# Optimization experiments

Measured on AMD Instinct MI355X. Metric: run time of the kernel, lower is better.

The kernel has to match this reference:

```python
import jax, jax.numpy as jnp
import numpy as np

IN1, IN2, OUT = 256, 64, 64

def setup_inputs() -> dict:
    key = jax.random.key(0)
    k1, k2, k3, k4 = jax.random.split(key, 4)
    x1 = jax.random.normal(k1, (4, 4096, IN1), dtype=jnp.float32)
    x2 = jax.random.normal(k2, (4, 4096, IN2), dtype=jnp.float32)
    # nn.Linear(in_1, in_2*out): weight (in_2*out, in_1), bias (in_2*out,)
    W = jax.random.normal(k3, (IN2 * OUT, IN1), dtype=jnp.float32) / np.sqrt(IN1)
    bvec = jax.random.normal(k4, (IN2 * OUT,), dtype=jnp.float32) * 0.01
    return {"x1": x1, "x2": x2, "W": W, "bvec": bvec}

def reference(x1, x2, W, bvec):
    b, n, _ = x1.shape
    # per-token generated weight: (b, n, in_2, out)
    w = (jnp.einsum('bni,oi->bno', x1, W) + bvec).reshape(b, n, IN2, OUT)
    # batched vector-matrix product per token
    y = jnp.einsum('bnj,bnjo->bno', x2, w)
    return y
```

## Files before the change

kernel.cpp:

```cpp
#include <hip/hip_runtime.h>


#define FRAGS 16
#define FRAG_SHORTS 512
#define JF_SHORTS (FRAGS * FRAG_SHORTS)
#define BIAS_OFF ((size_t)(64 * 2 * FRAGS) * FRAG_SHORTS)

typedef __bf16 bf16x8 __attribute__((ext_vector_type(8)));
typedef float  f32x16 __attribute__((ext_vector_type(16)));

static __device__ __forceinline__ unsigned short f2bf(float f) {
  union { float f; unsigned u; } v; v.f = f;
  unsigned r = v.u + 0x7FFFu + ((v.u >> 16) & 1u);
  return (unsigned short)(r >> 16);
}

static __device__ __forceinline__ void gload_lds16(const unsigned short* g,
                                                   unsigned short* l) {
  __builtin_amdgcn_global_load_lds(
      (const __attribute__((address_space(1))) void*)g,
      (__attribute__((address_space(3))) void*)l, 16, 0, 0);
}

__global__ void prep_w(const float* __restrict__ W, const float* __restrict__ bv,
                       unsigned short* __restrict__ Wf) {
  int idx = blockIdx.x * 256 + threadIdx.x;
  int r  = idx >> 4;
  int ks = idx & 15;
  int j   = r >> 6;
  int o   = r & 63;
  int oh  = o >> 5;
  int l31 = o & 31;
  size_t fb = ((size_t)(j * 2 + oh) * FRAGS + ks) * FRAG_SHORTS;

  const float4* row = (const float4*)(W + (size_t)r * 256 + ks * 16);
  float4 v0 = row[0], v1 = row[1], v2 = row[2], v3 = row[3];
  ushort4 lo0, lo1, hi0, hi1;
  lo0.x = f2bf(v0.x); lo0.y = f2bf(v0.y); lo0.z = f2bf(v0.z); lo0.w = f2bf(v0.w);
  lo1.x = f2bf(v1.x); lo1.y = f2bf(v1.y); lo1.z = f2bf(v1.z); lo1.w = f2bf(v1.w);
  hi0.x = f2bf(v2.x); hi0.y = f2bf(v2.y); hi0.z = f2bf(v2.z); hi0.w = f2bf(v2.w);
  hi1.x = f2bf(v3.x); hi1.y = f2bf(v3.y); hi1.z = f2bf(v3.z); hi1.w = f2bf(v3.w);
  *(ushort4*)&Wf[fb + l31 * 8 + 0] = lo0;
  *(ushort4*)&Wf[fb + l31 * 8 + 4] = lo1;
  *(ushort4*)&Wf[fb + 256 + l31 * 8 + 0] = hi0;
  *(ushort4*)&Wf[fb + 256 + l31 * 8 + 4] = hi1;

  if (idx < 512) {
    int f   = idx >> 6;
    int ln  = idx & 63;
    int ohb = f >> 2, jhb = f & 3;
    int lb  = ln & 31, lgb = ln >> 5;
    #pragma unroll
    for (int e = 0; e < 8; ++e)
      Wf[BIAS_OFF + (size_t)f * FRAG_SHORTS + ln * 8 + e] =
          f2bf(bv[(jhb * 16 + 8 * lgb + e) * 64 + 32 * ohb + lb]);
  }
}

__global__ __launch_bounds__(512, 2)
void meta_main(const float* __restrict__ x1, const float* __restrict__ x2,
               const unsigned short* __restrict__ Wf, float* __restrict__ out) {
  __shared__ __align__(16) unsigned char smem[163840];
  unsigned short* sWf = (unsigned short*)smem;
  float* sX2 = (float*)(smem + 131072);

  const int tid  = threadIdx.x;
  const int lane = tid & 63;
  const int wv   = tid >> 6;
  const int th   = wv & 1;
  const int jh   = wv >> 1;
  const int l31  = lane & 31;
  const int lg   = lane >> 5;

  const int bid  = blockIdx.x;
  const int xcd  = bid & 7;
  const int kk   = bid >> 3;
  const int tile = xcd * 16 + (kk >> 1);
  const int oh   = kk & 1;
  const long tile0 = (long)tile * 128;

  {
    const float4* src = (const float4*)(x1 + tile0 * 256);
    #pragma unroll
    for (int it = 0; it < 16; ++it) {
      int fi4 = it * 512 + tid;
      float4 v = src[fi4];
      int token = fi4 >> 6;
      int col   = (fi4 & 63) * 4;
      ushort4 b;
      b.x = f2bf(v.x); b.y = f2bf(v.y); b.z = f2bf(v.z); b.w = f2bf(v.w);
      *(ushort4*)&sWf[token * 264 + col] = b;
    }
    const float4* s2 = (const float4*)(x2 + tile0 * 64);
    #pragma unroll
    for (int it = 0; it < 4; ++it) {
      int fi4 = it * 512 + tid;
      float4 v = s2[fi4];
      int token = fi4 >> 4;
      int j0    = (fi4 & 15) * 4;
      sX2[(j0 + 0) * 128 + token] = v.x;
      sX2[(j0 + 1) * 128 + token] = v.y;
      sX2[(j0 + 2) * 128 + token] = v.z;
      sX2[(j0 + 3) * 128 + token] = v.w;
    }
  }
  __syncthreads();

  const int tA = th * 64 + l31;
  const int tB = tA + 32;

  bf16x8 bfA[16], bfB[16];
  #pragma unroll
  for (int ks = 0; ks < 16; ++ks) {
    bfA[ks] = *(const bf16x8*)&sWf[tA * 264 + ks * 16 + lg * 8];
    bfB[ks] = *(const bf16x8*)&sWf[tB * 264 + ks * 16 + lg * 8];
  }

  f32x16 yA, yB;
  {
    union { bf16x8 v; unsigned short u[8]; } xfA, xfB;
    #pragma unroll
    for (int e = 0; e < 8; ++e) {
      int jrow = jh * 16 + 8 * lg + e;
      xfA.u[e] = f2bf(sX2[jrow * 128 + tA]);
      xfB.u[e] = f2bf(sX2[jrow * 128 + tB]);
    }
    bf16x8 biasA = *(const bf16x8*)(Wf + BIAS_OFF +
                                    (size_t)(oh * 4 + jh) * FRAG_SHORTS + lane * 8);
    f32x16 z;
    #pragma unroll
    for (int r2 = 0; r2 < 16; ++r2) z[r2] = 0.0f;
    yA = __builtin_amdgcn_mfma_f32_32x32x16_bf16(biasA, xfA.v, z, 0, 0, 0);
    yB = __builtin_amdgcn_mfma_f32_32x32x16_bf16(biasA, xfB.v, z, 0, 0, 0);
  }
  __syncthreads();

  unsigned short* ring = sWf + jh * (2 * JF_SHORTS);
  const int ks0 = th * 8;

  {
    const unsigned short* src =
        Wf + ((size_t)((jh * 16) * 2 + oh) * FRAGS + ks0) * FRAG_SHORTS + lane * 8;
    unsigned short* dst = ring + ks0 * FRAG_SHORTS;
    #pragma unroll
    for (int q = 0; q < 8; ++q)
      gload_lds16(src + q * FRAG_SHORTS, dst + q * FRAG_SHORTS);
  }
  __syncthreads();

  #pragma unroll 2
  for (int i = 0; i < 16; ++i) {
    const int buf = i & 1;
    if (i + 1 < 16) {
      const int jn = jh * 16 + i + 1;
      const unsigned short* src =
          Wf + ((size_t)(jn * 2 + oh) * FRAGS + ks0) * FRAG_SHORTS + lane * 8;
      unsigned short* dst = ring + (buf ^ 1) * JF_SHORTS + ks0 * FRAG_SHORTS;
      #pragma unroll
      for (int q = 0; q < 8; ++q)
        gload_lds16(src + q * FRAG_SHORTS, dst + q * FRAG_SHORTS);
    }
    const unsigned short* rb = ring + buf * JF_SHORTS + lane * 8;
    f32x16 aA, aB;
    #pragma unroll
    for (int r2 = 0; r2 < 16; ++r2) { aA[r2] = 0.0f; aB[r2] = 0.0f; }
    #pragma unroll
    for (int ks = 0; ks < 16; ++ks) {
      bf16x8 wk = *(const bf16x8*)(rb + ks * FRAG_SHORTS);
      aA = __builtin_amdgcn_mfma_f32_32x32x16_bf16(wk, bfA[ks], aA, 0, 0, 0);
      aB = __builtin_amdgcn_mfma_f32_32x32x16_bf16(wk, bfB[ks], aB, 0, 0, 0);
    }
    const int j = jh * 16 + i;
    const float xA = sX2[j * 128 + tA];
    const float xB = sX2[j * 128 + tB];
    #pragma unroll
    for (int r2 = 0; r2 < 16; ++r2) {
      yA[r2] += xA * aA[r2];
      yB[r2] += xB * aB[r2];
    }
    __syncthreads();
  }

  float* red = (float*)sWf;
  const int sA = ((th * 2 + 0) * 64 + lane) * 4 + jh;
  const int sB = ((th * 2 + 1) * 64 + lane) * 4 + jh;
  if (jh != 0) {
    #pragma unroll
    for (int r2 = 0; r2 < 16; ++r2) {
      red[sA * 17 + r2] = yA[r2];
      red[sB * 17 + r2] = yB[r2];
    }
  }
  __syncthreads();
  if (jh == 0) {
    #pragma unroll
    for (int r2 = 0; r2 < 16; ++r2) {
      yA[r2] += red[(sA + 1) * 17 + r2] + red[(sA + 2) * 17 + r2] + red[(sA + 3) * 17 + r2];
      yB[r2] += red[(sB + 1) * 17 + r2] + red[(sB + 2) * 17 + r2] + red[(sB + 3) * 17 + r2];
    }
    float* yoA = out + (tile0 + tA) * 64 + oh * 32;
    float* yoB = out + (tile0 + tB) * 64 + oh * 32;
    #pragma unroll
    for (int rq = 0; rq < 4; ++rq) {
      float4 vA = make_float4(yA[4 * rq + 0], yA[4 * rq + 1], yA[4 * rq + 2], yA[4 * rq + 3]);
      float4 vB = make_float4(yB[4 * rq + 0], yB[4 * rq + 1], yB[4 * rq + 2], yB[4 * rq + 3]);
      *(float4*)(yoA + 8 * rq + 4 * lg) = vA;
      *(float4*)(yoB + 8 * rq + 4 * lg) = vB;
    }
  }
}

extern "C" void kernel_launch(void* const* d_in, const int* in_sizes, int n_in,
                              void* d_out, int out_size, void* d_ws, size_t ws_size,
                              hipStream_t stream) {
  const float* x1 = (const float*)d_in[0];
  const float* x2 = (const float*)d_in[1];
  const float* W  = (const float*)d_in[2];
  const float* bv = (const float*)d_in[3];
  float* y = (float*)d_out;
  unsigned short* Wf = (unsigned short*)d_ws;

  prep_w<<<256, 256, 0, stream>>>(W, bv, Wf);
  meta_main<<<256, 512, 0, stream>>>(x1, x2, Wf, y);
}
```

Baseline: 105.6 us.

## Split K across waves with register-streamed W fragments and tree reduction

Rewrites the main kernel's work split: each wave now owns a quarter of the K dimension and half of the j range, covering all 128 tokens. It loads x1 fragments straight from global into registers and streams the bf16 W fragments from global with register double-buffering, replacing the LDS ring fed by global_load_lds and its per-iteration barriers. Partial sums are combined through a multi-step LDS tree reduction. The aim is to cut barrier and LDS traffic and reuse each W fragment across more tokens, at the cost of more reduction work, higher register pressure, and dropping the XCD-aware tile mapping.

```diff
diff --git a/kernel.cpp b/kernel.cpp
--- a/kernel.cpp
+++ b/kernel.cpp
@@ -1,10 +1,9 @@
 #include <hip/hip_runtime.h>
 
 
-#define FRAGS 16
 #define FRAG_SHORTS 512
-#define JF_SHORTS (FRAGS * FRAG_SHORTS)
-#define BIAS_OFF ((size_t)(64 * 2 * FRAGS) * FRAG_SHORTS)
+#define JSTEP (2 * 16 * FRAG_SHORTS)
+#define BIAS_OFF ((size_t)(64 * 2 * 16) * FRAG_SHORTS)
 
 typedef __bf16 bf16x8 __attribute__((ext_vector_type(8)));
 typedef float  f32x16 __attribute__((ext_vector_type(16)));
@@ -15,11 +14,11 @@
   return (unsigned short)(r >> 16);
 }
 
-static __device__ __forceinline__ void gload_lds16(const unsigned short* g,
-                                                   unsigned short* l) {
-  __builtin_amdgcn_global_load_lds(
-      (const __attribute__((address_space(1))) void*)g,
-      (__attribute__((address_space(3))) void*)l, 16, 0, 0);
+static __device__ __forceinline__ bf16x8 pack8(float4 a, float4 b) {
+  union { bf16x8 v; unsigned short u[8]; } r;
+  r.u[0] = f2bf(a.x); r.u[1] = f2bf(a.y); r.u[2] = f2bf(a.z); r.u[3] = f2bf(a.w);
+  r.u[4] = f2bf(b.x); r.u[5] = f2bf(b.y); r.u[6] = f2bf(b.z); r.u[7] = f2bf(b.w);
+  return r.v;
 }
 
 __global__ void prep_w(const float* __restrict__ W, const float* __restrict__ bv,
@@ -31,7 +30,7 @@
   int o   = r & 63;
   int oh  = o >> 5;
   int l31 = o & 31;
-  size_t fb = ((size_t)(j * 2 + oh) * FRAGS + ks) * FRAG_SHORTS;
+  size_t fb = ((size_t)(j * 2 + oh) * 16 + ks) * FRAG_SHORTS;
 
   const float4* row = (const float4*)(W + (size_t)r * 256 + ks * 16);
   float4 v0 = row[0], v1 = row[1], v2 = row[2], v3 = row[3];
@@ -48,49 +47,35 @@
   if (idx < 512) {
     int f   = idx >> 6;
     int ln  = idx & 63;
-    int ohb = f >> 2, jhb = f & 3;
+    int ohb = f >> 2, jq = f & 3;
     int lb  = ln & 31, lgb = ln >> 5;
     #pragma unroll
     for (int e = 0; e < 8; ++e)
       Wf[BIAS_OFF + (size_t)f * FRAG_SHORTS + ln * 8 + e] =
-          f2bf(bv[(jhb * 16 + 8 * lgb + e) * 64 + 32 * ohb + lb]);
+          f2bf(bv[(jq * 16 + 8 * lgb + e) * 64 + 32 * ohb + lb]);
   }
 }
 
 __global__ __launch_bounds__(512, 2)
 void meta_main(const float* __restrict__ x1, const float* __restrict__ x2,
                const unsigned short* __restrict__ Wf, float* __restrict__ out) {
-  __shared__ __align__(16) unsigned char smem[163840];
-  unsigned short* sWf = (unsigned short*)smem;
-  float* sX2 = (float*)(smem + 131072);
+  __shared__ __align__(16) unsigned char smem[102400];
+  float* sX2 = (float*)smem;
+  float* red = (float*)(smem + 32768);
 
   const int tid  = threadIdx.x;
   const int lane = tid & 63;
   const int wv   = tid >> 6;
-  const int th   = wv & 1;
-  const int jh   = wv >> 1;
+  const int kh   = wv & 3;
+  const int jh   = wv >> 2;
   const int l31  = lane & 31;
   const int lg   = lane >> 5;
 
   const int bid  = blockIdx.x;
-  const int xcd  = bid & 7;
-  const int kk   = bid >> 3;
-  const int tile = xcd * 16 + (kk >> 1);
-  const int oh   = kk & 1;
-  const long tile0 = (long)tile * 128;
+  const int oh   = bid & 1;
+  const long tile0 = (long)(bid >> 1) * 128;
 
   {
-    const float4* src = (const float4*)(x1 + tile0 * 256);
-    #pragma unroll
-    for (int it = 0; it < 16; ++it) {
-      int fi4 = it * 512 + tid;
-      float4 v = src[fi4];
-      int token = fi4 >> 6;
-      int col   = (fi4 & 63) * 4;
-      ushort4 b;
-      b.x = f2bf(v.x); b.y = f2bf(v.y); b.z = f2bf(v.z); b.w = f2bf(v.w);
-      *(ushort4*)&sWf[token * 264 + col] = b;
-    }
     const float4* s2 = (const float4*)(x2 + tile0 * 64);
     #pragma unroll
     for (int it = 0; it < 4; ++it) {
@@ -104,110 +89,137 @@
       sX2[(j0 + 3) * 128 + token] = v.w;
     }
   }
-  __syncthreads();
-
-  const int tA = th * 64 + l31;
-  const int tB = tA + 32;
-
-  bf16x8 bfA[16], bfB[16];
-  #pragma unroll
-  for (int ks = 0; ks < 16; ++ks) {
-    bfA[ks] = *(const bf16x8*)&sWf[tA * 264 + ks * 16 + lg * 8];
-    bfB[ks] = *(const bf16x8*)&sWf[tB * 264 + ks * 16 + lg * 8];
-  }
-
-  f32x16 yA, yB;
-  {
-    union { bf16x8 v; unsigned short u[8]; } xfA, xfB;
-    #pragma unroll
-    for (int e = 0; e < 8; ++e) {
-      int jrow = jh * 16 + 8 * lg + e;
-      xfA.u[e] = f2bf(sX2[jrow * 128 + tA]);
-      xfB.u[e] = f2bf(sX2[jrow * 128 + tB]);
-    }
-    bf16x8 biasA = *(const bf16x8*)(Wf + BIAS_OFF +
-                                    (size_t)(oh * 4 + jh) * FRAG_SHORTS + lane * 8);
-    f32x16 z;
-    #pragma unroll
-    for (int r2 = 0; r2 < 16; ++r2) z[r2] = 0.0f;
-    yA = __builtin_amdgcn_mfma_f32_32x32x16_bf16(biasA, xfA.v, z, 0, 0, 0);
-    yB = __builtin_amdgcn_mfma_f32_32x32x16_bf16(biasA, xfB.v, z, 0, 0, 0);
-  }
-  __syncthreads();
-
-  unsigned short* ring = sWf + jh * (2 * JF_SHORTS);
-  const int ks0 = th * 8;
-
-  {
-    const unsigned short* src =
-        Wf + ((size_t)((jh * 16) * 2 + oh) * FRAGS + ks0) * FRAG_SHORTS + lane * 8;
-    unsigned short* dst = ring + ks0 * FRAG_SHORTS;
-    #pragma unroll
-    for (int q = 0; q < 8; ++q)
-      gload_lds16(src + q * FRAG_SHORTS, dst + q * FRAG_SHORTS);
-  }
-  __syncthreads();
-
-  #pragma unroll 2
-  for (int i = 0; i < 16; ++i) {
-    const int buf = i & 1;
-    if (i + 1 < 16) {
-      const int jn = jh * 16 + i + 1;
-      const unsigned short* src =
-          Wf + ((size_t)(jn * 2 + oh) * FRAGS + ks0) * FRAG_SHORTS + lane * 8;
-      unsigned short* dst = ring + (buf ^ 1) * JF_SHORTS + ks0 * FRAG_SHORTS;
+
+  bf16x8 bf[4][4];
+  #pragma unroll
+  for (int m = 0; m < 4; ++m) {
+    #pragma unroll
+    for (int q = 0; q < 4; ++q) {
+      const float* p = x1 + (size_t)(tile0 + m * 32 + l31) * 256 +
+                       (kh * 4 + q) * 16 + lg * 8;
+      bf[m][q] = pack8(*(const float4*)p, *(const float4*)(p + 4));
+    }
+  }
+  __syncthreads();
+
+  f32x16 z;
+  #pragma unroll
+  for (int r = 0; r < 16; ++r) z[r] = 0.0f;
+
+  f32x16 y[4];
+  #pragma unroll
+  for (int m = 0; m < 4; ++m) y[m] = z;
+  if (kh == 0) {
+    #pragma unroll
+    for (int qq = 0; qq < 2; ++qq) {
+      int jq = jh * 2 + qq;
+      bf16x8 bias = *(const bf16x8*)(Wf + BIAS_OFF +
+                                     (size_t)(oh * 4 + jq) * FRAG_SHORTS + lane * 8);
       #pragma unroll
-      for (int q = 0; q < 8; ++q)
-        gload_lds16(src + q * FRAG_SHORTS, dst + q * FRAG_SHORTS);
-    }
-    const unsigned short* rb = ring + buf * JF_SHORTS + lane * 8;
-    f32x16 aA, aB;
-    #pragma unroll
-    for (int r2 = 0; r2 < 16; ++r2) { aA[r2] = 0.0f; aB[r2] = 0.0f; }
-    #pragma unroll
-    for (int ks = 0; ks < 16; ++ks) {
-      bf16x8 wk = *(const bf16x8*)(rb + ks * FRAG_SHORTS);
-      aA = __builtin_amdgcn_mfma_f32_32x32x16_bf16(wk, bfA[ks], aA, 0, 0, 0);
-      aB = __builtin_amdgcn_mfma_f32_32x32x16_bf16(wk, bfB[ks], aB, 0, 0, 0);
-    }
-    const int j = jh * 16 + i;
-    const float xA = sX2[j * 128 + tA];
-    const float xB = sX2[j * 128 + tB];
-    #pragma unroll
-    for (int r2 = 0; r2 < 16; ++r2) {
-      yA[r2] += xA * aA[r2];
-      yB[r2] += xB * aB[r2];
-    }
-    __syncthreads();
-  }
-
-  float* red = (float*)sWf;
-  const int sA = ((th * 2 + 0) * 64 + lane) * 4 + jh;
-  const int sB = ((th * 2 + 1) * 64 + lane) * 4 + jh;
-  if (jh != 0) {
-    #pragma unroll
-    for (int r2 = 0; r2 < 16; ++r2) {
-      red[sA * 17 + r2] = yA[r2];
-      red[sB * 17 + r2] = yB[r2];
-    }
-  }
-  __syncthreads();
-  if (jh == 0) {
-    #pragma unroll
-    for (int r2 = 0; r2 < 16; ++r2) {
-      yA[r2] += red[(sA + 1) * 17 + r2] + red[(sA + 2) * 17 + r2] + red[(sA + 3) * 17 + r2];
-      yB[r2] += red[(sB + 1) * 17 + r2] + red[(sB + 2) * 17 + r2] + red[(sB + 3) * 17 + r2];
-    }
-    float* yoA = out + (tile0 + tA) * 64 + oh * 32;
-    float* yoB = out + (tile0 + tB) * 64 + oh * 32;
-    #pragma unroll
-    for (int rq = 0; rq < 4; ++rq) {
-      float4 vA = make_float4(yA[4 * rq + 0], yA[4 * rq + 1], yA[4 * rq + 2], yA[4 * rq + 3]);
-      float4 vB = make_float4(yB[4 * rq + 0], yB[4 * rq + 1], yB[4 * rq + 2], yB[4 * rq + 3]);
-      *(float4*)(yoA + 8 * rq + 4 * lg) = vA;
-      *(float4*)(yoB + 8 * rq + 4 * lg) = vB;
-    }
-  }
+      for (int m = 0; m < 4; ++m) {
+        union { bf16x8 v; unsigned short u[8]; } xf;
+        #pragma unroll
+        for (int e = 0; e < 8; ++e)
+          xf.u[e] = f2bf(sX2[(jq * 16 + 8 * lg + e) * 128 + m * 32 + l31]);
+        y[m] = __builtin_amdgcn_mfma_f32_32x32x16_bf16(bias, xf.v, y[m], 0, 0, 0);
+      }
+    }
+  }
+
+  const unsigned short* wp =
+      Wf + ((size_t)(jh * 32 * 2 + oh) * 16 + kh * 4) * FRAG_SHORTS + lane * 8;
+  bf16x8 wa[4], wb[4];
+  #pragma unroll
+  for (int q = 0; q < 4; ++q)
+    wa[q] = *(const bf16x8*)(wp + q * FRAG_SHORTS);
+
+#define COMPUTE(WREG, J)                                                        \
+  {                                                                             \
+    f32x16 aA, aB;                                                              \
+    aA = __builtin_amdgcn_mfma_f32_32x32x16_bf16(WREG[0], bf[0][0], z, 0, 0, 0);\
+    aB = __builtin_amdgcn_mfma_f32_32x32x16_bf16(WREG[0], bf[1][0], z, 0, 0, 0);\
+    aA = __builtin_amdgcn_mfma_f32_32x32x16_bf16(WREG[1], bf[0][1], aA, 0, 0, 0);\
+    aB = __builtin_amdgcn_mfma_f32_32x32x16_bf16(WREG[1], bf[1][1], aB, 0, 0, 0);\
+    aA = __builtin_amdgcn_mfma_f32_32x32x16_bf16(WREG[2], bf[0][2], aA, 0, 0, 0);\
+    aB = __builtin_amdgcn_mfma_f32_32x32x16_bf16(WREG[2], bf[1][2], aB, 0, 0, 0);\
+    aA = __builtin_amdgcn_mfma_f32_32x32x16_bf16(WREG[3], bf[0][3], aA, 0, 0, 0);\
+    aB = __builtin_amdgcn_mfma_f32_32x32x16_bf16(WREG[3], bf[1][3], aB, 0, 0, 0);\
+    float xs0 = sX2[(J) * 128 + l31];                                           \
+    float xs1 = sX2[(J) * 128 + 32 + l31];                                      \
+    _Pragma("unroll")                                                           \
+    for (int r = 0; r < 16; ++r) {                                              \
+      y[0][r] += xs0 * aA[r];                                                   \
+      y[1][r] += xs1 * aB[r];                                                   \
+    }                                                                           \
+    aA = __builtin_amdgcn_mfma_f32_32x32x16_bf16(WREG[0], bf[2][0], z, 0, 0, 0);\
+    aB = __builtin_amdgcn_mfma_f32_32x32x16_bf16(WREG[0], bf[3][0], z, 0, 0, 0);\
+    aA = __builtin_amdgcn_mfma_f32_32x32x16_bf16(WREG[1], bf[2][1], aA, 0, 0, 0);\
+    aB = __builtin_amdgcn_mfma_f32_32x32x16_bf16(WREG[1], bf[3][1], aB, 0, 0, 0);\
+    aA = __builtin_amdgcn_mfma_f32_32x32x16_bf16(WREG[2], bf[2][2], aA, 0, 0, 0);\
+    aB = __builtin_amdgcn_mfma_f32_32x32x16_bf16(WREG[2], bf[3][2], aB, 0, 0, 0);\
+    aA = __builtin_amdgcn_mfma_f32_32x32x16_bf16(WREG[3], bf[2][3], aA, 0, 0, 0);\
+    aB = __builtin_amdgcn_mfma_f32_32x32x16_bf16(WREG[3], bf[3][3], aB, 0, 0, 0);\
+    float xs2 = sX2[(J) * 128 + 64 + l31];                                      \
+    float xs3 = sX2[(J) * 128 + 96 + l31];                                      \
+    _Pragma("unroll")                                                           \
+    for (int r = 0; r < 16; ++r) {                                              \
+      y[2][r] += xs2 * aA[r];                                                   \
+      y[3][r] += xs3 * aB[r];                                                   \
+    }                                                                           \
+  }
+
+  for (int i = 0; i < 32; i += 2) {
+    const int jg = jh * 32 + i;
+    #pragma unroll
+    for (int q = 0; q < 4; ++q)
+      wb[q] = *(const bf16x8*)(wp + JSTEP + q * FRAG_SHORTS);
+    COMPUTE(wa, jg);
+    if (i + 2 < 32) {
+      #pragma unroll
+      for (int q = 0; q < 4; ++q)
+        wa[q] = *(const bf16x8*)(wp + 2 * JSTEP + q * FRAG_SHORTS);
+    }
+    COMPUTE(wb, jg + 1);
+    wp += 2 * JSTEP;
+  }
+#undef COMPUTE
+
+#define RED_W(S)                                                   \
+  { float* b = red + (S) * 4352;                                   \
+    _Pragma("unroll") for (int m = 0; m < 4; ++m)                  \
+      _Pragma("unroll") for (int r = 0; r < 16; ++r)               \
+        b[(m * 64 + lane) * 17 + r] = y[m][r]; }
+#define RED_A(S)                                                   \
+  { const float* b = red + (S) * 4352;                             \
+    _Pragma("unroll") for (int m = 0; m < 4; ++m)                  \
+      _Pragma("unroll") for (int r = 0; r < 16; ++r)               \
+        y[m][r] += b[(m * 64 + lane) * 17 + r]; }
+
+  if (kh >= 2) RED_W((kh - 2) * 2 + jh);
+  __syncthreads();
+  if (kh < 2)  RED_A(kh * 2 + jh);
+  __syncthreads();
+  if (kh == 1) RED_W(jh);
+  __syncthreads();
+  if (kh == 0) RED_A(jh);
+  __syncthreads();
+  if (kh == 0 && jh == 1) RED_W(0);
+  __syncthreads();
+  if (wv == 0) {
+    RED_A(0);
+    #pragma unroll
+    for (int m = 0; m < 4; ++m) {
+      float* yo = out + (tile0 + m * 32 + l31) * 64 + oh * 32;
+      #pragma unroll
+      for (int rq = 0; rq < 4; ++rq) {
+        float4 v = make_float4(y[m][4 * rq + 0], y[m][4 * rq + 1],
+                               y[m][4 * rq + 2], y[m][4 * rq + 3]);
+        *(float4*)(yo + 8 * rq + 4 * lg) = v;
+      }
+    }
+  }
+#undef RED_W
+#undef RED_A
 }
 
 extern "C" void kernel_launch(void* const* d_in, const int* in_sizes, int n_in,
```

Result: slower. 111.0 us (+5.1%).
